# Optimization experiments

Hardware: AMD Instinct MI355X
Metric: run time of the kernel (lower is better)

Reference implementation:

```python
import jax, jax.numpy as jnp
import numpy as np

B, T, S, D = 4, 16, 256, 1024
H, HKV = 16, 4
HD = D // H  # 64
N_IMG = 240  # image tokens; remaining S-N_IMG are agent tokens
LOGIT_CAP = 50.0
EPS = 1e-6


def _build_mask():
    # modality-aware mask: image tokens see only image tokens; agent tokens see all
    m = np.zeros((S, S), dtype=bool)
    m[:N_IMG, :N_IMG] = True
    m[N_IMG:, :] = True
    return jnp.asarray(m)


def _build_rope(s, hd):
    half = hd // 2
    inv_freq = 1.0 / (10000.0 ** (np.arange(half, dtype=np.float32) / half))
    pos = np.arange(s, dtype=np.float32)
    ang = np.outer(pos, inv_freq)  # (S, hd/2)
    return jnp.asarray(np.cos(ang)), jnp.asarray(np.sin(ang))


def setup_inputs() -> dict:
    key = jax.random.key(0)
    ks = jax.random.split(key, 7)
    rope_cos, rope_sin = _build_rope(S, HD)
    sc = 0.02
    return {
        "x": jax.random.normal(ks[0], (B, T, S, D), jnp.float32),
        "attn_mask": _build_mask(),
        "rope_cos": rope_cos,
        "rope_sin": rope_sin,
        "Wq": jax.random.normal(ks[1], (D, H * HD), jnp.float32) * sc,
        "Wk": jax.random.normal(ks[2], (D, HKV * HD), jnp.float32) * sc,
        "Wv": jax.random.normal(ks[3], (D, HKV * HD), jnp.float32) * sc,
        "Wo": jax.random.normal(ks[4], (D, D), jnp.float32) * sc,
        "q_scale": jnp.ones((HD,), jnp.float32),
        "k_scale": jnp.ones((HD,), jnp.float32),
    }


def _rmsnorm(t, scale):
    # RMSNorm over head_dim
    var = jnp.mean(jnp.square(t), axis=-1, keepdims=True)
    return t * jax.lax.rsqrt(var + EPS) * scale


def _rope(t, cos, sin):
    # rotate-half RoPE; t: (N, S, h, hd), cos/sin: (S, hd/2)
    half = t.shape[-1] // 2
    t1, t2 = t[..., :half], t[..., half:]
    c = cos[None, :, None, :]
    s = sin[None, :, None, :]
    return jnp.concatenate([t1 * c - t2 * s, t2 * c + t1 * s], axis=-1)


def reference(x, attn_mask, rope_cos, rope_sin, Wq, Wk, Wv, Wo, q_scale, k_scale):
    b, t, s, d = x.shape
    n = b * t
    xf = x.reshape(n, s, d)
    q = (xf @ Wq).reshape(n, s, H, HD)
    k = (xf @ Wk).reshape(n, s, HKV, HD)
    v = (xf @ Wv).reshape(n, s, HKV, HD)
    # QK-norm then RoPE
    q = _rope(_rmsnorm(q, q_scale), rope_cos, rope_sin)
    k = _rope(_rmsnorm(k, k_scale), rope_cos, rope_sin)
    # GQA: repeat kv heads
    rep = H // HKV
    k = jnp.repeat(k, rep, axis=2)
    v = jnp.repeat(v, rep, axis=2)
    scale = 1.0 / jnp.sqrt(jnp.asarray(HD, x.dtype))
    scores = jnp.einsum('nqhd,nkhd->nhqk', q, k) * scale
    # logit soft-capping
    scores = LOGIT_CAP * jnp.tanh(scores / LOGIT_CAP)
    big_neg = jnp.asarray(jnp.finfo(scores.dtype).min, scores.dtype)
    scores = jnp.where(attn_mask[None, None], scores, big_neg)
    p = jax.nn.softmax(scores, axis=-1)
    out = jnp.einsum('nhqk,nkhd->nqhd', p, v).reshape(n, s, d)
    return (out @ Wo).reshape(b, t, s, d)
```

## Files before the change

kernel.cpp:

```cpp
#include <hip/hip_runtime.h>

typedef __bf16 v8bf __attribute__((ext_vector_type(8)));
typedef __bf16 v4bf __attribute__((ext_vector_type(4)));
typedef float floatx4 __attribute__((ext_vector_type(4)));

#define MFMA16(a, b, c) __builtin_amdgcn_mfma_f32_16x16x32_bf16(a, b, c, 0, 0, 0)
#define GLL16(gp, lp)                                                        \
    __builtin_amdgcn_global_load_lds(                                        \
        (const __attribute__((address_space(1))) void*)(gp),                 \
        (__attribute__((address_space(3))) void*)(lp), 16, 0, 0)
#define VMW(n) asm volatile("s_waitcnt vmcnt(" #n ")" ::: "memory")
#define BARRIER() asm volatile("s_barrier" ::: "memory")

__global__ void prep(const float* __restrict__ x, __bf16* __restrict__ xb, int n4,
                     const float* __restrict__ W0, const float* __restrict__ W1,
                     const float* __restrict__ W2, const float* __restrict__ W3,
                     __bf16* __restrict__ dqkv, __bf16* __restrict__ dwo) {
    __shared__ __bf16 tile[64][65];
    int b = blockIdx.x;
    if (b < 640) {
        int k0 = (b & 15) * 64;
        int byy = b >> 4;
        bool isO = byy >= 24;
        int c0 = (isO ? byy - 24 : byy) * 64;
        for (int i = threadIdx.x; i < 4096; i += 256) {
            int k = i >> 6, c = i & 63;
            int gc = c0 + c;
            float v;
            if (isO)            v = W3[(k0 + k) * 1024 + gc];
            else if (gc < 1024) v = W0[(k0 + k) * 1024 + gc];
            else if (gc < 1280) v = W1[(k0 + k) * 256 + gc - 1024];
            else                v = W2[(k0 + k) * 256 + gc - 1280];
            tile[c][k] = (__bf16)v;
        }
        __syncthreads();
        __bf16* dst = isO ? dwo : dqkv;
        for (int i = threadIdx.x; i < 4096; i += 256) {
            int c = i >> 6, k = i & 63;
            dst[(c0 + c) * 1024 + k0 + k] = tile[c][k];
        }
    } else {
        int i = (b - 640) * 256 + threadIdx.x;
        int stride = (gridDim.x - 640) * 256;
        for (; i < n4; i += stride) {
            float4 v = ((const float4*)x)[i];
            v4bf o;
            o[0] = (__bf16)v.x; o[1] = (__bf16)v.y; o[2] = (__bf16)v.z; o[3] = (__bf16)v.w;
            ((v4bf*)xb)[i] = o;
        }
    }
}

template <typename OUT>
__global__ __launch_bounds__(256, 2) void gemm_bt(const __bf16* __restrict__ A,
                                                  const __bf16* __restrict__ B,
                                                  OUT* __restrict__ C, int N) {
    constexpr int SLAB = (128 + 256) * 32;
    __shared__ __attribute__((aligned(16))) __bf16 smem[3 * SLAB];
    const int t = threadIdx.x, lane = t & 63, w = t >> 6;
    const int gx = gridDim.x;
    const int nwg = gx * gridDim.y;
    const int id = blockIdx.y * gx + blockIdx.x;
    const int swz = (id & 7) * (nwg >> 3) + (id >> 3);
    const int m0 = (swz / gx) * 128, n0 = (swz % gx) * 256;
    const int wn = w * 64;
    const int rl = lane >> 2;
    const int gl = (lane & 3) ^ ((lane >> 3) & 3);
    const __bf16* pA = A + (long)(m0 + w * 32 + rl) * 1024 + gl * 8;
    const __bf16* pB = B + (long)(n0 + w * 64 + rl) * 1024 + gl * 8;
    const int lr = lane & 15, quad = lane >> 4, m = lane & 15;
    const int ga = ((quad ^ ((lr >> 1) & 3)) * 8);
    floatx4 acc[8][4] = {};

    auto STAGE = [&](int s) {
        __bf16* base = smem + (s % 3) * SLAB;
        const __bf16* sa = pA + s * 32;
        const __bf16* sb = pB + s * 32;
        GLL16(sa,             base + w * 1024);
        GLL16(sa + 16 * 1024, base + w * 1024 + 512);
        __bf16* bb = base + 4096;
        GLL16(sb,             bb + w * 2048);
        GLL16(sb + 16 * 1024, bb + w * 2048 + 512);
        GLL16(sb + 32 * 1024, bb + w * 2048 + 1024);
        GLL16(sb + 48 * 1024, bb + w * 2048 + 1536);
    };
    auto COMPUTE = [&](int s) {
        const __bf16* As_ = smem + (s % 3) * SLAB;
        const __bf16* Bs_ = As_ + 4096;
        v8bf af[8], bq[4];
#pragma unroll
        for (int i = 0; i < 8; ++i)
            af[i] = *(const v8bf*)(As_ + (i * 16 + lr) * 32 + ga);
#pragma unroll
        for (int j = 0; j < 4; ++j)
            bq[j] = *(const v8bf*)(Bs_ + (wn + j * 16 + lr) * 32 + ga);
        __builtin_amdgcn_s_setprio(1);
#pragma unroll
        for (int i = 0; i < 8; ++i)
#pragma unroll
            for (int j = 0; j < 4; ++j)
                acc[i][j] = MFMA16(af[i], bq[j], acc[i][j]);
        __builtin_amdgcn_s_setprio(0);
    };

    STAGE(0); STAGE(1);
#pragma unroll 1
    for (int s = 0; s < 30; ++s) {
        STAGE(s + 2);
        VMW(12);
        BARRIER();
        COMPUTE(s);
        BARRIER();
    }
    VMW(6);  BARRIER(); COMPUTE(30); BARRIER();
    VMW(0);  BARRIER(); COMPUTE(31);
    __syncthreads();

    const int row2 = lane >> 2, cb = lane & 3;
    if constexpr (sizeof(OUT) == 2) {
        __bf16* tile = smem + w * (16 * 68);
#pragma unroll
        for (int i = 0; i < 8; ++i) {
#pragma unroll
            for (int j = 0; j < 4; ++j)
#pragma unroll
                for (int r = 0; r < 4; ++r)
                    tile[(quad * 4 + r) * 68 + j * 16 + m] = (__bf16)acc[i][j][r];
            __bf16* dst = (__bf16*)C + (long)(m0 + i * 16 + row2) * N + n0 + wn + cb * 16;
            *(v8bf*)dst = *(const v8bf*)(&tile[row2 * 68 + cb * 16]);
            *(v8bf*)(dst + 8) = *(const v8bf*)(&tile[row2 * 68 + cb * 16 + 8]);
        }
    } else {
        float* tile = (float*)smem + w * (16 * 66);
#pragma unroll
        for (int i = 0; i < 8; ++i) {
#pragma unroll
            for (int j = 0; j < 4; ++j)
#pragma unroll
                for (int r = 0; r < 4; ++r)
                    tile[(quad * 4 + r) * 66 + j * 16 + m] = acc[i][j][r];
            float* dst = (float*)C + (long)(m0 + i * 16 + row2) * N + n0 + wn + cb * 16;
#pragma unroll
            for (int c = 0; c < 4; ++c)
                *(floatx4*)(dst + c * 4) = *(const floatx4*)(&tile[row2 * 66 + cb * 16 + c * 4]);
        }
    }
}

__global__ __launch_bounds__(512) void attn_kernel(const __bf16* __restrict__ qkv,
                                                   const float* __restrict__ rc,
                                                   const float* __restrict__ rs,
                                                   const float* __restrict__ qsc,
                                                   const float* __restrict__ ksc,
                                                   __bf16* __restrict__ O) {
    __shared__ __attribute__((aligned(16))) __bf16 KV[256 * 64];
    __shared__ __attribute__((aligned(16))) __bf16 Ps[8][16][40];
    const int bx = blockIdx.x;
    const int n = bx >> 5, h = (bx >> 1) & 15, half = bx & 1, hk = h >> 2;
    const int t = threadIdx.x, lane = t & 63, w = t >> 6;
    const int m = lane & 15, quad = lane >> 4;

    for (int p = 0; p < 4; ++p) {
        int l = t + p * 512;
        int s = l >> 3, cg = l & 7;
        v8bf kv = *(const v8bf*)(qkv + (long)(n * 256 + s) * 1536 + 1024 + hk * 64 + cg * 8);
        float f[8], ss2 = 0.f;
#pragma unroll
        for (int j = 0; j < 8; ++j) { f[j] = (float)kv[j]; ss2 += f[j] * f[j]; }
        ss2 += __shfl_xor(ss2, 1);
        ss2 += __shfl_xor(ss2, 2);
        ss2 += __shfl_xor(ss2, 4);
        float krr = rsqrtf(ss2 * (1.f / 64.f) + 1e-6f);
        float vs[8];
#pragma unroll
        for (int j = 0; j < 8; ++j) vs[j] = f[j] * krr * ksc[cg * 8 + j];
        v8bf outv;
#pragma unroll
        for (int j = 0; j < 8; ++j) {
            float pv = __shfl_xor(vs[j], 4);
            int hd = cg * 8 + j;
            float c = rc[s * 32 + (hd & 31)], sn = rs[s * 32 + (hd & 31)];
            outv[j] = (__bf16)((cg < 4) ? (vs[j] * c - pv * sn)
                                        : (vs[j] * c + pv * sn));
        }
        *(v8bf*)(&KV[s * 64 + ((cg ^ (s & 7)) * 8)]) = outv;
    }
    const int srow = half * 128 + w * 16 + m;
    const __bf16* qp = qkv + (long)(n * 256 + srow) * 1536 + h * 64 + quad * 8;
    v8bf qr0 = *(const v8bf*)(qp);
    v8bf qr1 = *(const v8bf*)(qp + 32);
    float f0[8], f1[8], ss = 0.f;
#pragma unroll
    for (int j = 0; j < 8; ++j) {
        f0[j] = (float)qr0[j]; f1[j] = (float)qr1[j];
        ss += f0[j] * f0[j] + f1[j] * f1[j];
    }
    ss += __shfl_xor(ss, 16);
    ss += __shfl_xor(ss, 32);
    float rr = rsqrtf(ss * (1.f / 64.f) + 1e-6f);
    v8bf qa0, qa1;
#pragma unroll
    for (int j = 0; j < 8; ++j) {
        int hd = quad * 8 + j;
        float t1 = f0[j] * rr * qsc[hd];
        float t2 = f1[j] * rr * qsc[32 + hd];
        float c = rc[srow * 32 + hd], sn = rs[srow * 32 + hd];
        qa0[j] = (__bf16)(t1 * c - t2 * sn);
        qa1[j] = (__bf16)(t2 * c + t1 * sn);
    }
    __syncthreads();

    floatx4 sc[16];
#pragma unroll
    for (int ti = 0; ti < 16; ++ti) {
        int kr = ti * 16 + m;
        v8bf b0 = *(const v8bf*)(&KV[kr * 64 + ((quad ^ (kr & 7)) * 8)]);
        v8bf b1 = *(const v8bf*)(&KV[kr * 64 + (((quad + 4) ^ (kr & 7)) * 8)]);
        floatx4 a = {0.f, 0.f, 0.f, 0.f};
        a = MFMA16(qa0, b0, a);
        a = MFMA16(qa1, b1, a);
        sc[ti] = a;
    }

    const int qbase = half * 128 + w * 16 + quad * 4;
    float sum[4] = {0.f, 0.f, 0.f, 0.f};
#pragma unroll
    for (int ti = 0; ti < 16; ++ti)
#pragma unroll
        for (int r = 0; r < 4; ++r) {
            float v = sc[ti][r];
            float e = __builtin_amdgcn_exp2f(v * 0.0072134752f);
            float capped = 50.f - 100.f * __builtin_amdgcn_rcpf(e + 1.f);
            float p = __builtin_amdgcn_exp2f(capped * 1.44269504f);
            if (ti == 15 && (qbase + r) < 240) p = 0.f;
            sc[ti][r] = p;
            sum[r] += p;
        }
    float inv[4];
#pragma unroll
    for (int r = 0; r < 4; ++r) {
#pragma unroll
        for (int msk = 1; msk < 16; msk <<= 1) sum[r] += __shfl_xor(sum[r], msk);
        inv[r] = __builtin_amdgcn_rcpf(sum[r]);
    }

    __syncthreads();
    for (int p = 0; p < 4; ++p) {
        int l = t + p * 512;
        int s = l >> 3, cg = l & 7;
        v8bf vv = *(const v8bf*)(qkv + (long)(n * 256 + s) * 1536 + 1280 + hk * 64 + cg * 8);
#pragma unroll
        for (int j = 0; j < 8; ++j)
            KV[(cg * 8 + j) * 256 + (((s >> 3) ^ j ^ cg) * 8) + (s & 7)] = vv[j];
    }
    __syncthreads();

    floatx4 oacc[4] = {};
#pragma unroll
    for (int kc = 0; kc < 8; ++kc) {
#pragma unroll
        for (int ht = 0; ht < 2; ++ht) {
            int ti = kc * 2 + ht;
#pragma unroll
            for (int r = 0; r < 4; ++r)
                Ps[w][quad * 4 + r][ht * 16 + m] = (__bf16)sc[ti][r];
        }
        v8bf pa = *(const v8bf*)(&Ps[w][m][quad * 8]);
#pragma unroll
        for (int ct = 0; ct < 4; ++ct) {
            int hd = ct * 16 + m;
            int sg = kc * 4 + quad;
            int sl = (sg ^ (hd & 7) ^ (hd >> 3)) & 31;
            v8bf vb = *(const v8bf*)(&KV[hd * 256 + sl * 8]);
            oacc[ct] = MFMA16(pa, vb, oacc[ct]);
        }
    }
#pragma unroll
    for (int ct = 0; ct < 4; ++ct)
#pragma unroll
        for (int r = 0; r < 4; ++r) {
            int qrow = half * 128 + w * 16 + quad * 4 + r;
            O[(long)(n * 256 + qrow) * 1024 + h * 64 + ct * 16 + m] =
                (__bf16)(oacc[ct][r] * inv[r]);
        }
}

extern "C" void kernel_launch(void* const* d_in, const int* in_sizes, int n_in,
                              void* d_out, int out_size, void* d_ws, size_t ws_size,
                              hipStream_t stream) {
    const float* x  = (const float*)d_in[0];
    const float* rc = (const float*)d_in[2];
    const float* rs = (const float*)d_in[3];
    const float* Wq = (const float*)d_in[4];
    const float* Wk = (const float*)d_in[5];
    const float* Wv = (const float*)d_in[6];
    const float* Wo = (const float*)d_in[7];
    const float* qs = (const float*)d_in[8];
    const float* ks = (const float*)d_in[9];
    float* out = (float*)d_out;
    char* ws = (char*)d_ws;

    __bf16* x_bf    = (__bf16*)(ws);
    __bf16* WqkvT   = (__bf16*)(ws + (32l << 20));
    __bf16* WoT     = (__bf16*)(ws + (35l << 20));
    __bf16* qkv_bf  = (__bf16*)(ws + (37l << 20));
    __bf16* attn_bf = (__bf16*)(ws + (93l << 20));

    prep<<<4736, 256, 0, stream>>>(x, x_bf, 16777216 / 4,
                                   Wq, Wk, Wv, Wo, WqkvT, WoT);
    gemm_bt<__bf16><<<dim3(6, 128), 256, 0, stream>>>(x_bf, WqkvT, qkv_bf, 1536);
    attn_kernel<<<2048, 512, 0, stream>>>(qkv_bf, rc, rs, qs, ks, attn_bf);
    gemm_bt<float><<<dim3(4, 128), 256, 0, stream>>>(attn_bf, WoT, out, 1024);
}
```

Before: 305.7 us.

## Fuse QK RMSNorm and RoPE into QKV GEMM epilogue

```diff
diff --git a/kernel.cpp b/kernel.cpp
--- a/kernel.cpp
+++ b/kernel.cpp
@@ -51,10 +51,14 @@
     }
 }
 
-template <typename OUT>
+template <bool NORM, typename OUT>
 __global__ __launch_bounds__(256, 2) void gemm_bt(const __bf16* __restrict__ A,
                                                   const __bf16* __restrict__ B,
-                                                  OUT* __restrict__ C, int N) {
+                                                  OUT* __restrict__ C, int N,
+                                                  const float* __restrict__ rc,
+                                                  const float* __restrict__ rs,
+                                                  const float* __restrict__ qsc,
+                                                  const float* __restrict__ ksc) {
     constexpr int SLAB = (128 + 256) * 32;
     __shared__ __attribute__((aligned(16))) __bf16 smem[3 * SLAB];
     const int t = threadIdx.x, lane = t & 63, w = t >> 6;
@@ -116,6 +120,42 @@
     VMW(0);  BARRIER(); COMPUTE(31);
     __syncthreads();
 
+    if constexpr (NORM) {
+        const int colbase = n0 + wn;
+        if (colbase < 1280) {
+            const float* sc_ = (colbase < 1024) ? qsc : ksc;
+            const float s0 = sc_[m],      s1 = sc_[16 + m];
+            const float s2 = sc_[32 + m], s3 = sc_[48 + m];
+#pragma unroll
+            for (int i = 0; i < 8; ++i) {
+                float sq[4];
+#pragma unroll
+                for (int r = 0; r < 4; ++r)
+                    sq[r] = acc[i][0][r] * acc[i][0][r] + acc[i][1][r] * acc[i][1][r]
+                          + acc[i][2][r] * acc[i][2][r] + acc[i][3][r] * acc[i][3][r];
+#pragma unroll
+                for (int msk = 1; msk < 16; msk <<= 1)
+#pragma unroll
+                    for (int r = 0; r < 4; ++r) sq[r] += __shfl_xor(sq[r], msk);
+#pragma unroll
+                for (int r = 0; r < 4; ++r) {
+                    float rrv = rsqrtf(sq[r] * (1.f / 64.f) + 1e-6f);
+                    int row = (m0 + i * 16 + quad * 4 + r) & 255;
+                    float c0 = rc[row * 32 + m],      sn0 = rs[row * 32 + m];
+                    float c1 = rc[row * 32 + 16 + m], sn1 = rs[row * 32 + 16 + m];
+                    float a0 = acc[i][0][r] * rrv * s0;
+                    float a1 = acc[i][1][r] * rrv * s1;
+                    float a2 = acc[i][2][r] * rrv * s2;
+                    float a3 = acc[i][3][r] * rrv * s3;
+                    acc[i][0][r] = a0 * c0 - a2 * sn0;
+                    acc[i][1][r] = a1 * c1 - a3 * sn1;
+                    acc[i][2][r] = a2 * c0 + a0 * sn0;
+                    acc[i][3][r] = a3 * c1 + a1 * sn1;
+                }
+            }
+        }
+    }
+
     const int row2 = lane >> 2, cb = lane & 3;
     if constexpr (sizeof(OUT) == 2) {
         __bf16* tile = smem + w * (16 * 68);
@@ -148,10 +188,6 @@
 }
 
 __global__ __launch_bounds__(512) void attn_kernel(const __bf16* __restrict__ qkv,
-                                                   const float* __restrict__ rc,
-                                                   const float* __restrict__ rs,
-                                                   const float* __restrict__ qsc,
-                                                   const float* __restrict__ ksc,
                                                    __bf16* __restrict__ O) {
     __shared__ __attribute__((aligned(16))) __bf16 KV[256 * 64];
     __shared__ __attribute__((aligned(16))) __bf16 Ps[8][16][40];
@@ -164,50 +200,12 @@
         int l = t + p * 512;
         int s = l >> 3, cg = l & 7;
         v8bf kv = *(const v8bf*)(qkv + (long)(n * 256 + s) * 1536 + 1024 + hk * 64 + cg * 8);
-        float f[8], ss2 = 0.f;
-#pragma unroll
-        for (int j = 0; j < 8; ++j) { f[j] = (float)kv[j]; ss2 += f[j] * f[j]; }
-        ss2 += __shfl_xor(ss2, 1);
-        ss2 += __shfl_xor(ss2, 2);
-        ss2 += __shfl_xor(ss2, 4);
-        float krr = rsqrtf(ss2 * (1.f / 64.f) + 1e-6f);
-        float vs[8];
-#pragma unroll
-        for (int j = 0; j < 8; ++j) vs[j] = f[j] * krr * ksc[cg * 8 + j];
-        v8bf outv;
-#pragma unroll
-        for (int j = 0; j < 8; ++j) {
-            float pv = __shfl_xor(vs[j], 4);
-            int hd = cg * 8 + j;
-            float c = rc[s * 32 + (hd & 31)], sn = rs[s * 32 + (hd & 31)];
-            outv[j] = (__bf16)((cg < 4) ? (vs[j] * c - pv * sn)
-                                        : (vs[j] * c + pv * sn));
-        }
-        *(v8bf*)(&KV[s * 64 + ((cg ^ (s & 7)) * 8)]) = outv;
+        *(v8bf*)(&KV[s * 64 + ((cg ^ (s & 7)) * 8)]) = kv;
     }
     const int srow = half * 128 + w * 16 + m;
     const __bf16* qp = qkv + (long)(n * 256 + srow) * 1536 + h * 64 + quad * 8;
-    v8bf qr0 = *(const v8bf*)(qp);
-    v8bf qr1 = *(const v8bf*)(qp + 32);
-    float f0[8], f1[8], ss = 0.f;
-#pragma unroll
-    for (int j = 0; j < 8; ++j) {
-        f0[j] = (float)qr0[j]; f1[j] = (float)qr1[j];
-        ss += f0[j] * f0[j] + f1[j] * f1[j];
-    }
-    ss += __shfl_xor(ss, 16);
-    ss += __shfl_xor(ss, 32);
-    float rr = rsqrtf(ss * (1.f / 64.f) + 1e-6f);
-    v8bf qa0, qa1;
-#pragma unroll
-    for (int j = 0; j < 8; ++j) {
-        int hd = quad * 8 + j;
-        float t1 = f0[j] * rr * qsc[hd];
-        float t2 = f1[j] * rr * qsc[32 + hd];
-        float c = rc[srow * 32 + hd], sn = rs[srow * 32 + hd];
-        qa0[j] = (__bf16)(t1 * c - t2 * sn);
-        qa1[j] = (__bf16)(t2 * c + t1 * sn);
-    }
+    v8bf qa0 = *(const v8bf*)(qp);
+    v8bf qa1 = *(const v8bf*)(qp + 32);
     __syncthreads();
 
     floatx4 sc[16];
@@ -230,8 +228,8 @@
         for (int r = 0; r < 4; ++r) {
             float v = sc[ti][r];
             float e = __builtin_amdgcn_exp2f(v * 0.0072134752f);
-            float capped = 50.f - 100.f * __builtin_amdgcn_rcpf(e + 1.f);
-            float p = __builtin_amdgcn_exp2f(capped * 1.44269504f);
+            float p = __builtin_amdgcn_exp2f(
+                fmaf(__builtin_amdgcn_rcpf(e + 1.f), -144.269504f, 72.134752f));
             if (ti == 15 && (qbase + r) < 240) p = 0.f;
             sc[ti][r] = p;
             sum[r] += p;
@@ -308,7 +306,9 @@
 
     prep<<<4736, 256, 0, stream>>>(x, x_bf, 16777216 / 4,
                                    Wq, Wk, Wv, Wo, WqkvT, WoT);
-    gemm_bt<__bf16><<<dim3(6, 128), 256, 0, stream>>>(x_bf, WqkvT, qkv_bf, 1536);
-    attn_kernel<<<2048, 512, 0, stream>>>(qkv_bf, rc, rs, qs, ks, attn_bf);
-    gemm_bt<float><<<dim3(4, 128), 256, 0, stream>>>(attn_bf, WoT, out, 1024);
+    gemm_bt<true, __bf16><<<dim3(6, 128), 256, 0, stream>>>(
+        x_bf, WqkvT, qkv_bf, 1536, rc, rs, qs, ks);
+    attn_kernel<<<2048, 512, 0, stream>>>(qkv_bf, attn_bf);
+    gemm_bt<false, float><<<dim3(4, 128), 256, 0, stream>>>(
+        attn_bf, WoT, out, 1024, nullptr, nullptr, nullptr, nullptr);
 }
```

Measured after the change: 310.6 us. No clear change (+1.6%).
